# Optimization experiments

Hardware: AMD Instinct MI355X
Metric: run time of the kernel (lower is better)

## Reference

```python
import jax, jax.numpy as jnp
import numpy as np

N_E = 1024
E_DIM = 64
BETA = 0.25


def setup_inputs() -> dict:
    key = jax.random.key(0)
    k1, k2 = jax.random.split(key)
    z = jax.random.normal(k1, (32, E_DIM, 32, 32), dtype=jnp.float32)
    embedding = jax.random.uniform(k2, (N_E, E_DIM), dtype=jnp.float32,
                                   minval=-1.0 / N_E, maxval=1.0 / N_E)
    return {"z": z, "embedding": embedding}


def reference(z, embedding):
    beta = BETA
    bt, ch, h, w = z.shape
    n_e = embedding.shape[0]
    # BCHW -> BHWC, flatten to [N, e_dim]
    zp = jnp.transpose(z, (0, 2, 3, 1))
    zf = zp.reshape(-1, ch)
    # squared L2 distances to each codebook entry: [N, n_e]
    d = (jnp.sum(zf ** 2, axis=1, keepdims=True)
         + jnp.sum(embedding ** 2, axis=1)
         - 2.0 * jnp.matmul(zf, embedding.T))
    idx = jnp.argmin(d, axis=1)                      # [N]
    min_encodings = jax.nn.one_hot(idx, n_e, dtype=jnp.float32)  # [N, n_e]
    # gather codebook rows (equivalent to one_hot @ embedding)
    z_q = embedding[idx].reshape(zp.shape)           # [B,H,W,C]
    loss = (jnp.mean((jax.lax.stop_gradient(z_q) - zp) ** 2)
            + beta * jnp.mean((z_q - jax.lax.stop_gradient(zp)) ** 2))
    # straight-through estimator
    z_q_st = zp + jax.lax.stop_gradient(z_q - zp)
    e_mean = jnp.mean(min_encodings, axis=0)
    perplexity = jnp.exp(-jnp.sum(e_mean * jnp.log(e_mean + 1e-10)))
    z_q_out = jnp.transpose(z_q_st, (0, 3, 1, 2))    # back to BCHW
    min_encoding_indices = idx.reshape(bt, h, w)
    return loss, z_q_out, perplexity, min_encodings, min_encoding_indices
```

## Files before the change

### kernel.cpp

```cpp
#include <hip/hip_runtime.h>
#include <cfloat>
#include <cstddef>


#define NROWS      32768
#define NE         1024
#define EDIM       64
#define RPB        64
#define NBLK       (NROWS / RPB)
#define TPB        512

#define OFF_LOSS   ((size_t)0)
#define OFF_ZQ     ((size_t)1)
#define OFF_PERP   ((size_t)2097153)
#define OFF_OH     ((size_t)2097154)
#define OFF_IDX    ((size_t)35651586)


__global__ __launch_bounds__(TPB, 4) void vq_main(const float* __restrict__ z,
                                                  const float* __restrict__ emb,
                                                  int* __restrict__ hist,
                                                  float* __restrict__ partial,
                                                  float* __restrict__ out) {
    const int t    = threadIdx.x;
    const int lane = t & 63;
    const int q    = t >> 6;
    const int r0   = blockIdx.x * RPB;
    const int row  = r0 + lane;
    const int b    = row >> 10;
    const int m    = row & 1023;
    const size_t zbase = (size_t)b * 65536 + (size_t)m;

    __shared__ float s_e2[NE];
    __shared__ float s_d[8][64];
    __shared__ int   s_j[8][64];
    __shared__ int   s_idx[64];
    __shared__ float s_l[8];

    for (int j = t; j < NE; j += TPB) {
        const float4* e4 = (const float4*)(emb + ((size_t)j << 6));
        double s = 0.0;
#pragma unroll
        for (int k = 0; k < 16; ++k) {
            float4 v = e4[k];
            s += (double)v.x * (double)v.x;
            s += (double)v.y * (double)v.y;
            s += (double)v.z * (double)v.z;
            s += (double)v.w * (double)v.w;
        }
        s_e2[j] = (float)s;
    }

    float4 zr[16];
#pragma unroll
    for (int k = 0; k < 16; ++k) {
        float4 v;
        v.x = z[zbase + (size_t)(4 * k + 0) * 1024];
        v.y = z[zbase + (size_t)(4 * k + 1) * 1024];
        v.z = z[zbase + (size_t)(4 * k + 2) * 1024];
        v.w = z[zbase + (size_t)(4 * k + 3) * 1024];
        zr[k] = v;
    }

    double z2d = 0.0;
#pragma unroll
    for (int k = 0; k < 16; ++k) {
        z2d += (double)zr[k].x * (double)zr[k].x;
        z2d += (double)zr[k].y * (double)zr[k].y;
        z2d += (double)zr[k].z * (double)zr[k].z;
        z2d += (double)zr[k].w * (double)zr[k].w;
    }
    const float z2f = (float)z2d;

    __syncthreads();

    const int jbase = __builtin_amdgcn_readfirstlane(q << 7);
    float bestd = FLT_MAX;
    int   bestj = NE;
    for (int jj = 0; jj < 128; jj += 2) {
        const int ja = jbase + jj;
        const int jb = ja + 1;
        const float4* ea = (const float4*)(emb + ((size_t)ja << 6));
        const float4* eb = (const float4*)(emb + ((size_t)jb << 6));
        float a0 = 0.f, a1 = 0.f, a2 = 0.f, a3 = 0.f;
        float b0 = 0.f, b1 = 0.f, b2 = 0.f, b3 = 0.f;
#pragma unroll
        for (int k = 0; k < 16; ++k) {
            float4 av = ea[k];
            float4 bv = eb[k];
            a0 = fmaf(av.x, zr[k].x, a0);
            a1 = fmaf(av.y, zr[k].y, a1);
            a2 = fmaf(av.z, zr[k].z, a2);
            a3 = fmaf(av.w, zr[k].w, a3);
            b0 = fmaf(bv.x, zr[k].x, b0);
            b1 = fmaf(bv.y, zr[k].y, b1);
            b2 = fmaf(bv.z, zr[k].z, b2);
            b3 = fmaf(bv.w, zr[k].w, b3);
        }
        float dota = (a0 + a1) + (a2 + a3);
        float dotb = (b0 + b1) + (b2 + b3);
        float da = (z2f + s_e2[ja]) - 2.0f * dota;
        float db = (z2f + s_e2[jb]) - 2.0f * dotb;
        if (da < bestd || (da == bestd && ja < bestj)) { bestd = da; bestj = ja; }
        if (db < bestd || (db == bestd && jb < bestj)) { bestd = db; bestj = jb; }
    }

    s_d[q][lane] = bestd;
    s_j[q][lane] = bestj;
    __syncthreads();
    if (t < 64) {
        float bd = s_d[0][t];
        int   bj = s_j[0][t];
#pragma unroll
        for (int w = 1; w < 8; ++w) {
            float dw = s_d[w][t];
            int   jw = s_j[w][t];
            if (dw < bd || (dw == bd && jw < bj)) { bd = dw; bj = jw; }
        }
        s_idx[t] = bj;
        out[OFF_IDX + (size_t)(r0 + t)] = (float)bj;
        atomicAdd(&hist[bj], 1);
    }
    __syncthreads();

    const int    jjx = s_idx[lane];
    const float* er  = emb + ((size_t)jjx << 6);
    float* zq = out + OFF_ZQ + (size_t)b * 65536 + (size_t)m;
    float lsum = 0.f;
#pragma unroll
    for (int c = q; c < EDIM; c += 8) {
        float zc   = z[zbase + (size_t)c * 1024];
        float ev   = er[c];
        float diff = ev - zc;
        zq[(size_t)c * 1024] = zc + diff;
        lsum = fmaf(diff, diff, lsum);
    }
#pragma unroll
    for (int off = 32; off >= 1; off >>= 1) lsum += __shfl_down(lsum, off);
    if (lane == 0) s_l[q] = lsum;
    __syncthreads();
    if (t == 0) {
        float l = 0.f;
#pragma unroll
        for (int w = 0; w < 8; ++w) l += s_l[w];
        partial[blockIdx.x] = l;
    }

    float* oh = out + OFF_OH;
    for (int mm = 0; mm < RPB; ++mm) {
        int    jr   = s_idx[mm];
        float* rowp = oh + (size_t)(r0 + mm) * 1024;
        float2 v0 = make_float2(0.f, 0.f);
        if ((jr >> 1) == t) ((float*)&v0)[jr & 1] = 1.0f;
        ((float2*)rowp)[t] = v0;
    }
}

__global__ __launch_bounds__(1024) void vq_final(const int* __restrict__ hist,
                                                 const float* __restrict__ partial,
                                                 float* __restrict__ out) {
    int t = threadIdx.x;
    float p    = (float)hist[t] * (1.0f / 32768.0f);
    float term = p * logf(p + 1e-10f);
    float lp   = (t < NBLK) ? partial[t] : 0.f;
#pragma unroll
    for (int off = 32; off >= 1; off >>= 1) {
        term += __shfl_down(term, off);
        lp   += __shfl_down(lp, off);
    }
    __shared__ float st[16], sl[16];
    int w = t >> 6, ln = t & 63;
    if (ln == 0) { st[w] = term; sl[w] = lp; }
    __syncthreads();
    if (t == 0) {
        float s = 0.f, l = 0.f;
#pragma unroll
        for (int i = 0; i < 16; ++i) { s += st[i]; l += sl[i]; }
        out[OFF_LOSS] = 1.25f * l * (1.0f / 2097152.0f);
        out[OFF_PERP] = expf(-s);
    }
}

extern "C" void kernel_launch(void* const* d_in, const int* in_sizes, int n_in,
                              void* d_out, int out_size, void* d_ws, size_t ws_size,
                              hipStream_t stream) {
    const float* z   = (const float*)d_in[0];
    const float* emb = (const float*)d_in[1];
    float* out     = (float*)d_out;
    int*   hist    = (int*)d_ws;
    float* partial = (float*)((char*)d_ws + 4096);

    hipMemsetAsync(hist, 0, 4096, stream);
    vq_main<<<NBLK, TPB, 0, stream>>>(z, emb, hist, partial, out);
    vq_final<<<1, 1024, 0, stream>>>(hist, partial, out);
}
```

Before: 256.2 us.

## Move histogram to final kernel, drop memset, use nontemporal one-hot stores

The codebook histogram is no longer built with global atomics in the main kernel. The final single-block kernel now rebuilds it in shared memory by reading back the written index output, which lets the separate memset launch go away. The one-hot matrix writes become nontemporal vector stores to avoid cache pollution on the large 128MB output, and an empty asm barrier pins the z registers loaded before the distance loop. The cost is that one block now serially reads 32K indices, which adds latency to the tail kernel.

After: 257.6 us. About the same (+0.5%).

```diff
diff --git a/kernel.cpp b/kernel.cpp
--- a/kernel.cpp
+++ b/kernel.cpp
@@ -16,10 +16,11 @@
 #define OFF_OH     ((size_t)2097154)
 #define OFF_IDX    ((size_t)35651586)
 
+typedef float f2_t __attribute__((ext_vector_type(2)));
+
 
 __global__ __launch_bounds__(TPB, 4) void vq_main(const float* __restrict__ z,
                                                   const float* __restrict__ emb,
-                                                  int* __restrict__ hist,
                                                   float* __restrict__ partial,
                                                   float* __restrict__ out) {
     const int t    = threadIdx.x;
@@ -60,6 +61,11 @@
         v.z = z[zbase + (size_t)(4 * k + 2) * 1024];
         v.w = z[zbase + (size_t)(4 * k + 3) * 1024];
         zr[k] = v;
+    }
+#pragma unroll
+    for (int k = 0; k < 16; ++k) {
+        asm volatile("" : "+v"(zr[k].x), "+v"(zr[k].y),
+                          "+v"(zr[k].z), "+v"(zr[k].w));
     }
 
     double z2d = 0.0;
@@ -119,7 +125,6 @@
         }
         s_idx[t] = bj;
         out[OFF_IDX + (size_t)(r0 + t)] = (float)bj;
-        atomicAdd(&hist[bj], 1);
     }
     __syncthreads();
 
@@ -150,17 +155,25 @@
     for (int mm = 0; mm < RPB; ++mm) {
         int    jr   = s_idx[mm];
         float* rowp = oh + (size_t)(r0 + mm) * 1024;
-        float2 v0 = make_float2(0.f, 0.f);
-        if ((jr >> 1) == t) ((float*)&v0)[jr & 1] = 1.0f;
-        ((float2*)rowp)[t] = v0;
+        f2_t v0 = (f2_t)(0.f);
+        if ((jr >> 1) == t) v0[jr & 1] = 1.0f;
+        __builtin_nontemporal_store(v0, (f2_t*)rowp + t);
     }
 }
 
-__global__ __launch_bounds__(1024) void vq_final(const int* __restrict__ hist,
-                                                 const float* __restrict__ partial,
+__global__ __launch_bounds__(1024) void vq_final(const float* __restrict__ partial,
                                                  float* __restrict__ out) {
-    int t = threadIdx.x;
-    float p    = (float)hist[t] * (1.0f / 32768.0f);
+    const int t = threadIdx.x;
+    __shared__ int   s_hist[NE];
+    __shared__ float st[16], sl[16];
+    s_hist[t] = 0;
+    __syncthreads();
+    const float* idxf = out + OFF_IDX;
+    for (int i = t; i < NROWS; i += 1024) {
+        atomicAdd(&s_hist[(int)idxf[i]], 1);
+    }
+    __syncthreads();
+    float p    = (float)s_hist[t] * (1.0f / 32768.0f);
     float term = p * logf(p + 1e-10f);
     float lp   = (t < NBLK) ? partial[t] : 0.f;
 #pragma unroll
@@ -168,7 +181,6 @@
         term += __shfl_down(term, off);
         lp   += __shfl_down(lp, off);
     }
-    __shared__ float st[16], sl[16];
     int w = t >> 6, ln = t & 63;
     if (ln == 0) { st[w] = term; sl[w] = lp; }
     __syncthreads();
@@ -187,10 +199,8 @@
     const float* z   = (const float*)d_in[0];
     const float* emb = (const float*)d_in[1];
     float* out     = (float*)d_out;
-    int*   hist    = (int*)d_ws;
-    float* partial = (float*)((char*)d_ws + 4096);
-
-    hipMemsetAsync(hist, 0, 4096, stream);
-    vq_main<<<NBLK, TPB, 0, stream>>>(z, emb, hist, partial, out);
-    vq_final<<<1, 1024, 0, stream>>>(hist, partial, out);
+    float* partial = (float*)d_ws;
+
+    vq_main<<<NBLK, TPB, 0, stream>>>(z, emb, partial, out);
+    vq_final<<<1, 1024, 0, stream>>>(partial, out);
 }
```

## Split embedding dim across half-waves and use nontemporal one-hot stores

Applied to the files above, without the earlier changes.

Each row's 64-channel dot product is now split between two half-waves of 32 channels, combined with a cross-half shuffle. This halves the z registers per thread (8 float4 instead of 16), aimed at higher occupancy. Each wave now scans 256 codes for 32 rows instead of 128 codes for 64 rows, and the argmin reduction is regrouped to match. The one-hot matrix is written with nontemporal stores to avoid polluting cache. The price is a shuffle per code pair and redundant emb loads across the two row groups.

Result: slower. 418.8 us (+63.4%).

```diff
diff --git a/kernel.cpp b/kernel.cpp
--- a/kernel.cpp
+++ b/kernel.cpp
@@ -15,6 +15,8 @@
 #define OFF_PERP   ((size_t)2097153)
 #define OFF_OH     ((size_t)2097154)
 #define OFF_IDX    ((size_t)35651586)
+
+typedef float f2_t __attribute__((ext_vector_type(2)));
 
 
 __global__ __launch_bounds__(TPB, 4) void vq_main(const float* __restrict__ z,
@@ -24,16 +26,21 @@
                                                   float* __restrict__ out) {
     const int t    = threadIdx.x;
     const int lane = t & 63;
-    const int q    = t >> 6;
+    const int wv   = t >> 6;
+    const int rgrp = wv >> 2;
+    const int wq   = wv & 3;
+    const int half = lane >> 5;
+    const int rr   = lane & 31;
     const int r0   = blockIdx.x * RPB;
-    const int row  = r0 + lane;
+    const int row  = r0 + rgrp * 32 + rr;
     const int b    = row >> 10;
     const int m    = row & 1023;
+    const int ch0  = half * 32;
     const size_t zbase = (size_t)b * 65536 + (size_t)m;
 
     __shared__ float s_e2[NE];
-    __shared__ float s_d[8][64];
-    __shared__ int   s_j[8][64];
+    __shared__ float s_d[8][32];
+    __shared__ int   s_j[8][32];
     __shared__ int   s_idx[64];
     __shared__ float s_l[8];
 
@@ -51,41 +58,47 @@
         s_e2[j] = (float)s;
     }
 
-    float4 zr[16];
-#pragma unroll
-    for (int k = 0; k < 16; ++k) {
+    float4 zr[8];
+#pragma unroll
+    for (int k = 0; k < 8; ++k) {
         float4 v;
-        v.x = z[zbase + (size_t)(4 * k + 0) * 1024];
-        v.y = z[zbase + (size_t)(4 * k + 1) * 1024];
-        v.z = z[zbase + (size_t)(4 * k + 2) * 1024];
-        v.w = z[zbase + (size_t)(4 * k + 3) * 1024];
+        v.x = z[zbase + (size_t)(ch0 + 4 * k + 0) * 1024];
+        v.y = z[zbase + (size_t)(ch0 + 4 * k + 1) * 1024];
+        v.z = z[zbase + (size_t)(ch0 + 4 * k + 2) * 1024];
+        v.w = z[zbase + (size_t)(ch0 + 4 * k + 3) * 1024];
         zr[k] = v;
     }
-
-    double z2d = 0.0;
-#pragma unroll
-    for (int k = 0; k < 16; ++k) {
-        z2d += (double)zr[k].x * (double)zr[k].x;
-        z2d += (double)zr[k].y * (double)zr[k].y;
-        z2d += (double)zr[k].z * (double)zr[k].z;
-        z2d += (double)zr[k].w * (double)zr[k].w;
-    }
-    const float z2f = (float)z2d;
-
-    __syncthreads();
-
-    const int jbase = __builtin_amdgcn_readfirstlane(q << 7);
+#pragma unroll
+    for (int k = 0; k < 8; ++k) {
+        asm volatile("" : "+v"(zr[k].x), "+v"(zr[k].y),
+                          "+v"(zr[k].z), "+v"(zr[k].w));
+    }
+
+    double z2h = 0.0;
+#pragma unroll
+    for (int k = 0; k < 8; ++k) {
+        z2h += (double)zr[k].x * (double)zr[k].x;
+        z2h += (double)zr[k].y * (double)zr[k].y;
+        z2h += (double)zr[k].z * (double)zr[k].z;
+        z2h += (double)zr[k].w * (double)zr[k].w;
+    }
+    const double z2o = __shfl_xor(z2h, 32);
+    const float  z2f = (float)(z2h + z2o);
+
+    __syncthreads();
+
+    const int jbase = __builtin_amdgcn_readfirstlane(wq << 8);
     float bestd = FLT_MAX;
     int   bestj = NE;
-    for (int jj = 0; jj < 128; jj += 2) {
+    for (int jj = 0; jj < 256; jj += 2) {
         const int ja = jbase + jj;
         const int jb = ja + 1;
-        const float4* ea = (const float4*)(emb + ((size_t)ja << 6));
-        const float4* eb = (const float4*)(emb + ((size_t)jb << 6));
+        const float4* ea = (const float4*)(emb + ((size_t)ja << 6) + ch0);
+        const float4* eb = (const float4*)(emb + ((size_t)jb << 6) + ch0);
         float a0 = 0.f, a1 = 0.f, a2 = 0.f, a3 = 0.f;
         float b0 = 0.f, b1 = 0.f, b2 = 0.f, b3 = 0.f;
 #pragma unroll
-        for (int k = 0; k < 16; ++k) {
+        for (int k = 0; k < 8; ++k) {
             float4 av = ea[k];
             float4 bv = eb[k];
             a0 = fmaf(av.x, zr[k].x, a0);
@@ -97,24 +110,28 @@
             b2 = fmaf(bv.z, zr[k].z, b2);
             b3 = fmaf(bv.w, zr[k].w, b3);
         }
-        float dota = (a0 + a1) + (a2 + a3);
-        float dotb = (b0 + b1) + (b2 + b3);
+        float pa = (a0 + a1) + (a2 + a3);
+        float pb = (b0 + b1) + (b2 + b3);
+        float dota = pa + __shfl_xor(pa, 32);
+        float dotb = pb + __shfl_xor(pb, 32);
         float da = (z2f + s_e2[ja]) - 2.0f * dota;
         float db = (z2f + s_e2[jb]) - 2.0f * dotb;
         if (da < bestd || (da == bestd && ja < bestj)) { bestd = da; bestj = ja; }
         if (db < bestd || (db == bestd && jb < bestj)) { bestd = db; bestj = jb; }
     }
 
-    s_d[q][lane] = bestd;
-    s_j[q][lane] = bestj;
+    if (half == 0) { s_d[wv][rr] = bestd; s_j[wv][rr] = bestj; }
     __syncthreads();
     if (t < 64) {
-        float bd = s_d[0][t];
-        int   bj = s_j[0][t];
-#pragma unroll
-        for (int w = 1; w < 8; ++w) {
-            float dw = s_d[w][t];
-            int   jw = s_j[w][t];
+        const int g   = t >> 5;
+        const int rr2 = t & 31;
+        const int w0  = g * 4;
+        float bd = s_d[w0][rr2];
+        int   bj = s_j[w0][rr2];
+#pragma unroll
+        for (int i = 1; i < 4; ++i) {
+            float dw = s_d[w0 + i][rr2];
+            int   jw = s_j[w0 + i][rr2];
             if (dw < bd || (dw == bd && jw < bj)) { bd = dw; bj = jw; }
         }
         s_idx[t] = bj;
@@ -123,13 +140,19 @@
     }
     __syncthreads();
 
-    const int    jjx = s_idx[lane];
-    const float* er  = emb + ((size_t)jjx << 6);
-    float* zq = out + OFF_ZQ + (size_t)b * 65536 + (size_t)m;
+    const int    ln64 = lane;
+    const int    q8   = wv;
+    const int    rowE = r0 + ln64;
+    const int    bE   = rowE >> 10;
+    const int    mE   = rowE & 1023;
+    const size_t zbE  = (size_t)bE * 65536 + (size_t)mE;
+    const int    jjx  = s_idx[ln64];
+    const float* er   = emb + ((size_t)jjx << 6);
+    float* zq = out + OFF_ZQ + (size_t)bE * 65536 + (size_t)mE;
     float lsum = 0.f;
 #pragma unroll
-    for (int c = q; c < EDIM; c += 8) {
-        float zc   = z[zbase + (size_t)c * 1024];
+    for (int c = q8; c < EDIM; c += 8) {
+        float zc   = z[zbE + (size_t)c * 1024];
         float ev   = er[c];
         float diff = ev - zc;
         zq[(size_t)c * 1024] = zc + diff;
@@ -137,7 +160,7 @@
     }
 #pragma unroll
     for (int off = 32; off >= 1; off >>= 1) lsum += __shfl_down(lsum, off);
-    if (lane == 0) s_l[q] = lsum;
+    if (lane == 0) s_l[q8] = lsum;
     __syncthreads();
     if (t == 0) {
         float l = 0.f;
@@ -150,16 +173,16 @@
     for (int mm = 0; mm < RPB; ++mm) {
         int    jr   = s_idx[mm];
         float* rowp = oh + (size_t)(r0 + mm) * 1024;
-        float2 v0 = make_float2(0.f, 0.f);
-        if ((jr >> 1) == t) ((float*)&v0)[jr & 1] = 1.0f;
-        ((float2*)rowp)[t] = v0;
+        f2_t v0 = (f2_t)(0.f);
+        if ((jr >> 1) == t) v0[jr & 1] = 1.0f;
+        __builtin_nontemporal_store(v0, (f2_t*)rowp + t);
     }
 }
 
 __global__ __launch_bounds__(1024) void vq_final(const int* __restrict__ hist,
                                                  const float* __restrict__ partial,
                                                  float* __restrict__ out) {
-    int t = threadIdx.x;
+    const int t = threadIdx.x;
     float p    = (float)hist[t] * (1.0f / 32768.0f);
     float term = p * logf(p + 1e-10f);
     float lp   = (t < NBLK) ? partial[t] : 0.f;
```

## Register-tile distance GEMM with packed FMA and shared-memory z staging

Applied to the files above, without the earlier changes.

The distance computation is restructured from one-row-per-thread dot products into an 8-row by 8-codeword register tile per thread. Each block stages its 64 z rows transposed in shared memory and uses packed two-wide FMA, with double-buffered codebook loads and shuffle-based argmin reductions. The block shrinks to 256 threads, and the one-hot writes become nontemporal stores. The aim is more reuse of each loaded value and higher FMA throughput, at the cost of more registers and therefore possibly lower occupancy.

Measured after the change: 781.3 us. 3.05x slower.

```diff
diff --git a/kernel.cpp b/kernel.cpp
--- a/kernel.cpp
+++ b/kernel.cpp
@@ -3,133 +3,184 @@
 #include <cstddef>
 
 
-#define NROWS      32768
-#define NE         1024
-#define EDIM       64
-#define RPB        64
-#define NBLK       (NROWS / RPB)
-#define TPB        512
-
-#define OFF_LOSS   ((size_t)0)
-#define OFF_ZQ     ((size_t)1)
-#define OFF_PERP   ((size_t)2097153)
-#define OFF_OH     ((size_t)2097154)
-#define OFF_IDX    ((size_t)35651586)
-
-
-__global__ __launch_bounds__(TPB, 4) void vq_main(const float* __restrict__ z,
+#define NROWS 32768
+#define NE    1024
+#define EDIM  64
+#define RPB   64
+#define NBLK  (NROWS / RPB)
+#define TPB   256
+
+#define OFF_LOSS ((size_t)0)
+#define OFF_ZQ   ((size_t)1)
+#define OFF_PERP ((size_t)2097153)
+#define OFF_OH   ((size_t)2097154)
+#define OFF_IDX  ((size_t)35651586)
+
+typedef float f2_t __attribute__((ext_vector_type(2)));
+
+
+__global__ __launch_bounds__(TPB, 2) void vq_main(const float* __restrict__ z,
                                                   const float* __restrict__ emb,
                                                   int* __restrict__ hist,
                                                   float* __restrict__ partial,
                                                   float* __restrict__ out) {
     const int t    = threadIdx.x;
     const int lane = t & 63;
-    const int q    = t >> 6;
+    const int w    = t >> 6;
+    const int rg   = lane >> 3;
+    const int cg   = lane & 7;
+    const int rb   = rg << 3;
     const int r0   = blockIdx.x * RPB;
-    const int row  = r0 + lane;
-    const int b    = row >> 10;
-    const int m    = row & 1023;
-    const size_t zbase = (size_t)b * 65536 + (size_t)m;
-
+    const int bb   = r0 >> 10;
+    const int m0   = r0 & 1023;
+
+    __shared__ float s_zT[64][64];
     __shared__ float s_e2[NE];
-    __shared__ float s_d[8][64];
-    __shared__ int   s_j[8][64];
+    __shared__ float s_z2[64];
+    __shared__ float s_wd[4][64];
+    __shared__ int   s_wj[4][64];
     __shared__ int   s_idx[64];
-    __shared__ float s_l[8];
-
-    for (int j = t; j < NE; j += TPB) {
+    __shared__ float s_l[4];
+
+    {
+        const int k = t >> 2, mg = t & 3;
+        const float* src = z + (size_t)bb * 65536 + (size_t)k * 1024 + (m0 + mg * 16);
+        float* dst = &s_zT[k][mg * 16];
+#pragma unroll
+        for (int i = 0; i < 4; ++i)
+            ((float4*)dst)[i] = ((const float4*)src)[i];
+    }
+#pragma unroll
+    for (int i = 0; i < 4; ++i) {
+        const int j = t + 256 * i;
         const float4* e4 = (const float4*)(emb + ((size_t)j << 6));
         double s = 0.0;
 #pragma unroll
         for (int k = 0; k < 16; ++k) {
             float4 v = e4[k];
-            s += (double)v.x * (double)v.x;
-            s += (double)v.y * (double)v.y;
-            s += (double)v.z * (double)v.z;
-            s += (double)v.w * (double)v.w;
+            s += (double)v.x * (double)v.x; s += (double)v.y * (double)v.y;
+            s += (double)v.z * (double)v.z; s += (double)v.w * (double)v.w;
         }
         s_e2[j] = (float)s;
     }
-
-    float4 zr[16];
-#pragma unroll
-    for (int k = 0; k < 16; ++k) {
-        float4 v;
-        v.x = z[zbase + (size_t)(4 * k + 0) * 1024];
-        v.y = z[zbase + (size_t)(4 * k + 1) * 1024];
-        v.z = z[zbase + (size_t)(4 * k + 2) * 1024];
-        v.w = z[zbase + (size_t)(4 * k + 3) * 1024];
-        zr[k] = v;
-    }
-
-    double z2d = 0.0;
-#pragma unroll
-    for (int k = 0; k < 16; ++k) {
-        z2d += (double)zr[k].x * (double)zr[k].x;
-        z2d += (double)zr[k].y * (double)zr[k].y;
-        z2d += (double)zr[k].z * (double)zr[k].z;
-        z2d += (double)zr[k].w * (double)zr[k].w;
-    }
-    const float z2f = (float)z2d;
-
-    __syncthreads();
-
-    const int jbase = __builtin_amdgcn_readfirstlane(q << 7);
-    float bestd = FLT_MAX;
-    int   bestj = NE;
-    for (int jj = 0; jj < 128; jj += 2) {
-        const int ja = jbase + jj;
-        const int jb = ja + 1;
-        const float4* ea = (const float4*)(emb + ((size_t)ja << 6));
-        const float4* eb = (const float4*)(emb + ((size_t)jb << 6));
-        float a0 = 0.f, a1 = 0.f, a2 = 0.f, a3 = 0.f;
-        float b0 = 0.f, b1 = 0.f, b2 = 0.f, b3 = 0.f;
-#pragma unroll
-        for (int k = 0; k < 16; ++k) {
-            float4 av = ea[k];
-            float4 bv = eb[k];
-            a0 = fmaf(av.x, zr[k].x, a0);
-            a1 = fmaf(av.y, zr[k].y, a1);
-            a2 = fmaf(av.z, zr[k].z, a2);
-            a3 = fmaf(av.w, zr[k].w, a3);
-            b0 = fmaf(bv.x, zr[k].x, b0);
-            b1 = fmaf(bv.y, zr[k].y, b1);
-            b2 = fmaf(bv.z, zr[k].z, b2);
-            b3 = fmaf(bv.w, zr[k].w, b3);
-        }
-        float dota = (a0 + a1) + (a2 + a3);
-        float dotb = (b0 + b1) + (b2 + b3);
-        float da = (z2f + s_e2[ja]) - 2.0f * dota;
-        float db = (z2f + s_e2[jb]) - 2.0f * dotb;
-        if (da < bestd || (da == bestd && ja < bestj)) { bestd = da; bestj = ja; }
-        if (db < bestd || (db == bestd && jb < bestj)) { bestd = db; bestj = jb; }
-    }
-
-    s_d[q][lane] = bestd;
-    s_j[q][lane] = bestj;
     __syncthreads();
     if (t < 64) {
-        float bd = s_d[0][t];
-        int   bj = s_j[0][t];
-#pragma unroll
-        for (int w = 1; w < 8; ++w) {
-            float dw = s_d[w][t];
-            int   jw = s_j[w][t];
-            if (dw < bd || (dw == bd && jw < bj)) { bd = dw; bj = jw; }
-        }
-        s_idx[t] = bj;
-        out[OFF_IDX + (size_t)(r0 + t)] = (float)bj;
-        atomicAdd(&hist[bj], 1);
-    }
-    __syncthreads();
-
+        double s = 0.0;
+        for (int k = 0; k < 64; ++k) {
+            float v = s_zT[k][t];
+            s += (double)v * (double)v;
+        }
+        s_z2[t] = (float)s;
+    }
+    __syncthreads();
+
+    f2_t z2p[4];
+#pragma unroll
+    for (int rq = 0; rq < 4; ++rq) {
+        z2p[rq][0] = s_z2[rb + 2 * rq];
+        z2p[rq][1] = s_z2[rb + 2 * rq + 1];
+    }
+
+    float bd[8]; int bj[8];
+#pragma unroll
+    for (int i = 0; i < 8; ++i) { bd[i] = FLT_MAX; bj[i] = NE; }
+
+    for (int cidx = 0; cidx < 4; ++cidx) {
+        const int c0 = ((cidx * 4 + w) << 6) + (cg << 3);
+        f2_t acc[8][4];
+#pragma unroll
+        for (int c = 0; c < 8; ++c)
+#pragma unroll
+            for (int rq = 0; rq < 4; ++rq) acc[c][rq] = (f2_t)(0.f);
+
+        auto fma_group = [&](const float4 (&ef)[8], int kbase) {
+#pragma unroll
+            for (int kk = 0; kk < 4; ++kk) {
+                const int k = kbase + kk;
+                const float4 zlo = *(const float4*)&s_zT[k][rb];
+                const float4 zhi = *(const float4*)&s_zT[k][rb + 4];
+                f2_t zp[4];
+                zp[0][0] = zlo.x; zp[0][1] = zlo.y;
+                zp[1][0] = zlo.z; zp[1][1] = zlo.w;
+                zp[2][0] = zhi.x; zp[2][1] = zhi.y;
+                zp[3][0] = zhi.z; zp[3][1] = zhi.w;
+#pragma unroll
+                for (int c = 0; c < 8; ++c) {
+                    const float sc = (&ef[c].x)[kk];
+                    const f2_t sv = {sc, sc};
+#pragma unroll
+                    for (int rq = 0; rq < 4; ++rq)
+                        acc[c][rq] = __builtin_elementwise_fma(zp[rq], sv, acc[c][rq]);
+                }
+            }
+        };
+
+        float4 ef0[8], ef1[8];
+#pragma unroll
+        for (int c = 0; c < 8; ++c)
+            ef0[c] = *(const float4*)(emb + ((size_t)(c0 + c) << 6));
+
+#pragma unroll 1
+        for (int k4 = 0; k4 < 16; k4 += 2) {
+#pragma unroll
+            for (int c = 0; c < 8; ++c)
+                ef1[c] = *(const float4*)(emb + ((size_t)(c0 + c) << 6) + ((k4 + 1) << 2));
+            fma_group(ef0, k4 << 2);
+#pragma unroll
+            for (int c = 0; c < 8; ++c)
+                ef0[c] = *(const float4*)(emb + ((size_t)(c0 + c) << 6) + (((k4 + 2) & 15) << 2));
+            fma_group(ef1, (k4 + 1) << 2);
+        }
+
+#pragma unroll
+        for (int c = 0; c < 8; ++c) {
+            const float e2c = s_e2[c0 + c];
+            const int   j   = c0 + c;
+#pragma unroll
+            for (int rq = 0; rq < 4; ++rq) {
+                f2_t d = (z2p[rq] + e2c) - 2.0f * acc[c][rq];
+                if (d[0] < bd[2 * rq])     { bd[2 * rq]     = d[0]; bj[2 * rq]     = j; }
+                if (d[1] < bd[2 * rq + 1]) { bd[2 * rq + 1] = d[1]; bj[2 * rq + 1] = j; }
+            }
+        }
+    }
+
+#pragma unroll
+    for (int mask = 1; mask < 8; mask <<= 1) {
+#pragma unroll
+        for (int i = 0; i < 8; ++i) {
+            float od = __shfl_xor(bd[i], mask);
+            int   oj = __shfl_xor(bj[i], mask);
+            if (od < bd[i] || (od == bd[i] && oj < bj[i])) { bd[i] = od; bj[i] = oj; }
+        }
+    }
+    if (cg == 0) {
+#pragma unroll
+        for (int i = 0; i < 8; ++i) { s_wd[w][rb + i] = bd[i]; s_wj[w][rb + i] = bj[i]; }
+    }
+    __syncthreads();
+
+    if (t < 64) {
+        float bdd = s_wd[0][t]; int bjj = s_wj[0][t];
+#pragma unroll
+        for (int ww = 1; ww < 4; ++ww) {
+            float dw = s_wd[ww][t]; int jw = s_wj[ww][t];
+            if (dw < bdd || (dw == bdd && jw < bjj)) { bdd = dw; bjj = jw; }
+        }
+        s_idx[t] = bjj;
+        out[OFF_IDX + (size_t)(r0 + t)] = (float)bjj;
+        atomicAdd(&hist[bjj], 1);
+    }
+    __syncthreads();
+
+    const size_t zbE = (size_t)bb * 65536 + (size_t)(m0 + lane);
     const int    jjx = s_idx[lane];
     const float* er  = emb + ((size_t)jjx << 6);
-    float* zq = out + OFF_ZQ + (size_t)b * 65536 + (size_t)m;
+    float* zq = out + OFF_ZQ + zbE;
     float lsum = 0.f;
 #pragma unroll
-    for (int c = q; c < EDIM; c += 8) {
-        float zc   = z[zbase + (size_t)c * 1024];
+    for (int c = w; c < EDIM; c += 4) {
+        float zc   = s_zT[c][lane];
         float ev   = er[c];
         float diff = ev - zc;
         zq[(size_t)c * 1024] = zc + diff;
@@ -137,29 +188,28 @@
     }
 #pragma unroll
     for (int off = 32; off >= 1; off >>= 1) lsum += __shfl_down(lsum, off);
-    if (lane == 0) s_l[q] = lsum;
-    __syncthreads();
-    if (t == 0) {
-        float l = 0.f;
-#pragma unroll
-        for (int w = 0; w < 8; ++w) l += s_l[w];
-        partial[blockIdx.x] = l;
-    }
+    if (lane == 0) s_l[w] = lsum;
+    __syncthreads();
+    if (t == 0)
+        partial[blockIdx.x] = (s_l[0] + s_l[1]) + (s_l[2] + s_l[3]);
 
     float* oh = out + OFF_OH;
     for (int mm = 0; mm < RPB; ++mm) {
-        int    jr   = s_idx[mm];
+        const int jr = s_idx[mm];
         float* rowp = oh + (size_t)(r0 + mm) * 1024;
-        float2 v0 = make_float2(0.f, 0.f);
-        if ((jr >> 1) == t) ((float*)&v0)[jr & 1] = 1.0f;
-        ((float2*)rowp)[t] = v0;
+        f2_t v0 = (f2_t)(0.f);
+        if ((jr >> 1) == t) v0[jr & 1] = 1.0f;
+        __builtin_nontemporal_store(v0, (f2_t*)rowp + t);
+        f2_t v1 = (f2_t)(0.f);
+        if ((jr >> 1) == t + 256) v1[jr & 1] = 1.0f;
+        __builtin_nontemporal_store(v1, (f2_t*)rowp + t + 256);
     }
 }
 
 __global__ __launch_bounds__(1024) void vq_final(const int* __restrict__ hist,
                                                  const float* __restrict__ partial,
                                                  float* __restrict__ out) {
-    int t = threadIdx.x;
+    const int t = threadIdx.x;
     float p    = (float)hist[t] * (1.0f / 32768.0f);
     float term = p * logf(p + 1e-10f);
     float lp   = (t < NBLK) ? partial[t] : 0.f;
@@ -169,8 +219,8 @@
         lp   += __shfl_down(lp, off);
     }
     __shared__ float st[16], sl[16];
-    int w = t >> 6, ln = t & 63;
-    if (ln == 0) { st[w] = term; sl[w] = lp; }
+    int ww = t >> 6, ln = t & 63;
+    if (ln == 0) { st[ww] = term; sl[ww] = lp; }
     __syncthreads();
     if (t == 0) {
         float s = 0.f, l = 0.f;
```
